# Kernel tuning notes

Measured on AMD Instinct MI355X. Metric: run time of the kernel, lower is better.

## Reference

```python
import jax, jax.numpy as jnp
import numpy as np

EPS = 1e-5


def _lstm(x, W_ih, W_hh, b_ih, b_hh):
    # x: [B, T, in]; torch LSTM gate order i, f, g, o. Returns (last h, last c).
    def step(carry, xt):
        h, c = carry
        z = xt @ W_ih.T + h @ W_hh.T + (b_ih + b_hh)  # [B, 4H]
        i, f, g, o = jnp.split(z, 4, axis=-1)
        c = jax.nn.sigmoid(f) * c + jax.nn.sigmoid(i) * jnp.tanh(g)
        h = jax.nn.sigmoid(o) * jnp.tanh(c)
        return (h, c), None
    h0 = jnp.zeros((x.shape[0], W_hh.shape[1]), x.dtype)
    (h, c), _ = jax.lax.scan(step, (h0, h0), jnp.swapaxes(x, 0, 1))
    return h, c


def _bn_train(x, g, b):
    # BatchNorm1d in training mode: batch stats, biased variance.
    m = x.mean(axis=0)
    v = x.var(axis=0)
    return g * (x - m) * jax.lax.rsqrt(v + EPS) + b


def _forward(agent_traj, neighbours, aW_ih, aW_hh, ab_ih, ab_hh,
             nW_ih, nW_hh, nb_ih, nb_hh, dW_ih, dW_hh, db_ih, db_hh,
             pW, pb, rW, rb, m1W, m1b, g1, be1, m2W, m2b, g2, be2,
             i1W, i1b, ig1, ib1, i2W, i2b, ig2, ib2, segment_ids):
    B = agent_traj.shape[0]
    # relative distance: neighbour last position - owning agent's last position
    rel = neighbours[:, -1, :] - agent_traj[segment_ids, -1, :]          # [N, 2]
    agent_h, agent_c = _lstm(agent_traj, aW_ih, aW_hh, ab_ih, ab_hh)     # [B, 64]
    neigh_h, _ = _lstm(neighbours, nW_ih, nW_hh, nb_ih, nb_hh)           # [N, 64]
    rel_emb = rel @ rW.T + rb                                            # [N, 64]
    x = jnp.concatenate([neigh_h, rel_emb], axis=1)                      # [N, 128]
    x = _bn_train(jax.nn.relu(x @ m1W.T + m1b), g1, be1)                 # [N, 512]
    x = _bn_train(jax.nn.relu(x @ m2W.T + m2b), g2, be2)                 # [N, 1024]
    # per-sample max pooling over each sample's neighbours (zeros if none)
    pooled = jax.ops.segment_max(x, segment_ids, num_segments=B)         # [B, 1024]
    counts = jax.ops.segment_sum(jnp.ones((x.shape[0],), x.dtype), segment_ids, num_segments=B)
    pooled = jnp.where(counts[:, None] > 0, pooled, jnp.zeros((), x.dtype))
    d = jnp.concatenate([pooled, agent_h], axis=1)                       # [B, 1088]
    d = _bn_train(jax.nn.relu(d @ i1W.T + i1b), ig1, ib1)                # [B, 1024]
    d = _bn_train(jax.nn.relu(d @ i2W.T + i2b), ig2, ib2)                # [B, 64]

    def dec_step(carry, _):
        h, c = carry
        z = h @ dW_ih.T + h @ dW_hh.T + (db_ih + db_hh)
        i, f, g, o = jnp.split(z, 4, axis=-1)
        c = jax.nn.sigmoid(f) * c + jax.nn.sigmoid(i) * jnp.tanh(g)
        h = jax.nn.sigmoid(o) * jnp.tanh(c)
        return (h, c), h
    _, hs = jax.lax.scan(dec_step, (d, agent_c), None, length=30)        # [30, B, 64]
    pred = jnp.einsum('tbh,oh->bto', hs, pW) + pb                        # [B, 30, 2]
    return pred


def setup_inputs() -> dict:
    B, T, N, Tn, H = 2048, 20, 32768, 20, 64
    key = jax.random.key(0)
    ki = iter(jax.random.split(key, 40))
    def rn(shape, s=0.1):
        return jax.random.normal(next(ki), shape, dtype=jnp.float32) * s
    inp = dict(
        agent_traj=rn((B, T, 2), 1.0),
        neighbours=rn((N, Tn, 2), 1.0),
        aW_ih=rn((4 * H, 2)), aW_hh=rn((4 * H, H)), ab_ih=rn((4 * H,)), ab_hh=rn((4 * H,)),
        nW_ih=rn((4 * H, 2)), nW_hh=rn((4 * H, H)), nb_ih=rn((4 * H,)), nb_hh=rn((4 * H,)),
        dW_ih=rn((4 * H, H)), dW_hh=rn((4 * H, H)), db_ih=rn((4 * H,)), db_hh=rn((4 * H,)),
        pW=rn((2, H)), pb=rn((2,)),
        rW=rn((H, 2)), rb=rn((H,)),
        m1W=rn((512, 128)), m1b=rn((512,)),
        g1=jnp.ones((512,), jnp.float32), be1=jnp.zeros((512,), jnp.float32),
        m2W=rn((1024, 512)), m2b=rn((1024,)),
        g2=jnp.ones((1024,), jnp.float32), be2=jnp.zeros((1024,), jnp.float32),
        i1W=rn((1024, 1088)), i1b=rn((1024,)),
        ig1=jnp.ones((1024,), jnp.float32), ib1=jnp.zeros((1024,), jnp.float32),
        i2W=rn((H, 1024)), i2b=rn((H,)),
        ig2=jnp.ones((H,), jnp.float32), ib2=jnp.zeros((H,), jnp.float32),
        segment_ids=jnp.sort(jax.random.randint(next(ki), (N,), 0, B)).astype(jnp.int32),
    )
    return inp


def reference(agent_traj, neighbours, aW_ih, aW_hh, ab_ih, ab_hh,
              nW_ih, nW_hh, nb_ih, nb_hh, dW_ih, dW_hh, db_ih, db_hh,
              pW, pb, rW, rb, m1W, m1b, g1, be1, m2W, m2b, g2, be2,
              i1W, i1b, ig1, ib1, i2W, i2b, ig2, ib2, segment_ids):
    return _forward(agent_traj, neighbours, aW_ih, aW_hh, ab_ih, ab_hh,
                    nW_ih, nW_hh, nb_ih, nb_hh, dW_ih, dW_hh, db_ih, db_hh,
                    pW, pb, rW, rb, m1W, m1b, g1, be1, m2W, m2b, g2, be2,
                    i1W, i1b, ig1, ib1, i2W, i2b, ig2, ib2, segment_ids)
```

## Files before the change

### kernel.cpp

```cpp
#include <hip/hip_runtime.h>

#define EPS_BN 1e-5f

typedef __attribute__((ext_vector_type(8))) short short8;
typedef __attribute__((ext_vector_type(4))) float f32x4;

__device__ __forceinline__ float fast_rcp(float x) { return __builtin_amdgcn_rcpf(x); }
__device__ __forceinline__ float sigmoid_f(float x) { return fast_rcp(1.0f + __expf(-x)); }
__device__ __forceinline__ float tanh_f(float x) { return 1.0f - 2.0f * fast_rcp(__expf(2.0f * x) + 1.0f); }

__device__ __forceinline__ unsigned short f2bf(float f) {
    unsigned u = __float_as_uint(f);
    u += 0x7FFFu + ((u >> 16) & 1u);
    return (unsigned short)(u >> 16);
}
__device__ __forceinline__ unsigned pk_bf(float a, float b) {
    return (unsigned)f2bf(a) | ((unsigned)f2bf(b) << 16);
}
__device__ __forceinline__ float bf_hi(float f) {
    return __uint_as_float((unsigned)f2bf(f) << 16);
}
__device__ __forceinline__ float bf2f(unsigned short u) {
    return __uint_as_float((unsigned)u << 16);
}

union AFrag { short e[8]; short8 v; };
union BFrag { uint4 u; short8 v; };

__global__ __launch_bounds__(256, 2) void lstm_mfma(
    const float* __restrict__ x,
    const float* __restrict__ W_ih,
    const float* __restrict__ W_hh,
    const float* __restrict__ b_ih,
    const float* __restrict__ b_hh,
    float* __restrict__ h_out,
    float* __restrict__ c_out,
    int T)
{
    __shared__ unsigned h_ex[2][2][16 * 52];

    const int tid  = threadIdx.x;
    const int w    = tid >> 6;
    const int lane = tid & 63;
    const int s    = lane & 15;
    const int q    = lane >> 4;

    short8 ahi[4][3], alo[4][3];
#pragma unroll
    for (int gt = 0; gt < 4; ++gt) {
        const int n = gt * 64 + w * 16 + s;
#pragma unroll
        for (int kc = 0; kc < 2; ++kc) {
            const float* src = &W_hh[n * 64 + kc * 32 + q * 8];
            float4 v0 = *(const float4*)src;
            float4 v1 = *(const float4*)(src + 4);
            float v[8] = {v0.x, v0.y, v0.z, v0.w, v1.x, v1.y, v1.z, v1.w};
            AFrag a, b;
#pragma unroll
            for (int j = 0; j < 8; ++j) {
                a.e[j] = (short)f2bf(v[j]);
                b.e[j] = (short)f2bf(v[j] - bf_hi(v[j]));
            }
            ahi[gt][kc] = a.v;
            alo[gt][kc] = b.v;
        }
        AFrag a2, b2;
#pragma unroll
        for (int j = 0; j < 8; ++j) { a2.e[j] = 0; b2.e[j] = 0; }
        if (q == 0) {
            const float wi0 = W_ih[n * 2 + 0];
            const float wi1 = W_ih[n * 2 + 1];
            const float bs  = b_ih[n] + b_hh[n];
            a2.e[0] = (short)f2bf(wi0); b2.e[0] = (short)f2bf(wi0 - bf_hi(wi0));
            a2.e[1] = (short)f2bf(wi1); b2.e[1] = (short)f2bf(wi1 - bf_hi(wi1));
            a2.e[2] = (short)f2bf(bs);  b2.e[2] = (short)f2bf(bs  - bf_hi(bs));
        }
        ahi[gt][2] = a2.v;
        alo[gt][2] = b2.v;
    }

    for (int i = tid; i < 2 * 2 * 16 * 52; i += 256) (&h_ex[0][0][0])[i] = 0u;
    __syncthreads();
    if (tid < 16) {
        h_ex[0][0][tid * 52 + 33] = pk_bf(1.0f, 0.0f);
        h_ex[1][0][tid * 52 + 33] = pk_bf(1.0f, 0.0f);
        float2 xv = *(const float2*)&x[((long)blockIdx.x * 16 + tid) * (long)(T * 2)];
        h_ex[0][0][tid * 52 + 32] = pk_bf(xv.x, xv.y);
        h_ex[0][1][tid * 52 + 32] = pk_bf(xv.x - bf_hi(xv.x), xv.y - bf_hi(xv.y));
    }
    __syncthreads();

    float creg[4] = {0.f, 0.f, 0.f, 0.f};

    for (int t = 0; t < T; ++t) {
        const int rb = t & 1, wb = rb ^ 1;
        BFrag bhi[3], blo[3];
#pragma unroll
        for (int kc = 0; kc < 3; ++kc) {
            const int off = s * 52 + kc * 16 + (q >> 1) * 8 + (q & 1) * 4;
            bhi[kc].u = *(const uint4*)&h_ex[rb][0][off];
            blo[kc].u = *(const uint4*)&h_ex[rb][1][off];
        }

        f32x4 acc[4];
#pragma unroll
        for (int gt = 0; gt < 4; ++gt) acc[gt] = (f32x4)0.f;

#pragma unroll
        for (int kc = 0; kc < 3; ++kc) {
            const short8 bh = bhi[kc].v;
            const short8 bl = blo[kc].v;
#pragma unroll
            for (int gt = 0; gt < 4; ++gt) {
                f32x4 a = acc[gt];
                a = __builtin_amdgcn_mfma_f32_16x16x32_bf16(ahi[gt][kc], bh, a, 0, 0, 0);
                a = __builtin_amdgcn_mfma_f32_16x16x32_bf16(ahi[gt][kc], bl, a, 0, 0, 0);
                a = __builtin_amdgcn_mfma_f32_16x16x32_bf16(alo[gt][kc], bh, a, 0, 0, 0);
                acc[gt] = a;
            }
        }

        float hval[4];
#pragma unroll
        for (int r = 0; r < 4; ++r) {
            const float c = fmaf(sigmoid_f(acc[1][r]), creg[r],
                                 sigmoid_f(acc[0][r]) * tanh_f(acc[2][r]));
            creg[r] = c;
            hval[r] = sigmoid_f(acc[3][r]) * tanh_f(c);
        }
        {
            const int w0 = s * 52 + w * 8 + q * 2;
            h_ex[wb][0][w0]     = pk_bf(hval[0], hval[1]);
            h_ex[wb][0][w0 + 1] = pk_bf(hval[2], hval[3]);
            h_ex[wb][1][w0]     = pk_bf(hval[0] - bf_hi(hval[0]), hval[1] - bf_hi(hval[1]));
            h_ex[wb][1][w0 + 1] = pk_bf(hval[2] - bf_hi(hval[2]), hval[3] - bf_hi(hval[3]));
        }
        if (tid < 16 && t + 1 < T) {
            float2 xv = *(const float2*)&x[((long)blockIdx.x * 16 + tid) * (long)(T * 2) + (t + 1) * 2];
            h_ex[wb][0][tid * 52 + 32] = pk_bf(xv.x, xv.y);
            h_ex[wb][1][tid * 52 + 32] = pk_bf(xv.x - bf_hi(xv.x), xv.y - bf_hi(xv.y));
        }
        if (t == T - 1) {
            const long seq = (long)blockIdx.x * 16 + s;
            const int j0 = w * 16 + q * 4;
            *(float4*)&h_out[seq * 64 + j0] = make_float4(hval[0], hval[1], hval[2], hval[3]);
            if (c_out)
                *(float4*)&c_out[seq * 64 + j0] = make_float4(creg[0], creg[1], creg[2], creg[3]);
        }
        __syncthreads();
    }
}

__global__ __launch_bounds__(256) void build_x0(
    const float* __restrict__ neigh_h, const float* __restrict__ neighbours,
    const float* __restrict__ agent_traj, const int* __restrict__ seg,
    const float* __restrict__ rW, const float* __restrict__ rb,
    unsigned short* __restrict__ x0hi, unsigned short* __restrict__ x0lo, int T)
{
    const long n = (long)blockIdx.x * 2 + (threadIdx.x >> 7);
    const int j = threadIdx.x & 127;
    float v;
    if (j < 64) {
        v = neigh_h[n*64 + j];
    } else {
        const int o = j - 64;
        const int sid = seg[n];
        const float ra = neighbours[n*(long)(T*2) + (T-1)*2 + 0] - agent_traj[(long)sid*(T*2) + (T-1)*2 + 0];
        const float rbv= neighbours[n*(long)(T*2) + (T-1)*2 + 1] - agent_traj[(long)sid*(T*2) + (T-1)*2 + 1];
        v = fmaf(rW[o*2+0], ra, fmaf(rW[o*2+1], rbv, rb[o]));
    }
    x0hi[n*128 + j] = f2bf(v);
    x0lo[n*128 + j] = f2bf(v - bf_hi(v));
}

__global__ __launch_bounds__(64) void prep_wfrag(
    const float* __restrict__ W, const float* __restrict__ sc, int K,
    unsigned short* __restrict__ Whi, unsigned short* __restrict__ Wlo)
{
    const int nKc = K >> 5;
    const int blk = blockIdx.x;
    const int ti = blk / nKc, kc = blk - ti * nKc;
    const int l = threadIdx.x;
    const int n = ti * 16 + (l & 15);
    const int k0 = kc * 32 + (l >> 4) * 8;
    const long ob = ((long)blk * 64 + l) * 8;
#pragma unroll
    for (int j = 0; j < 8; ++j) {
        float v = W[(long)n * K + k0 + j];
        if (sc) v *= sc[k0 + j];
        Whi[ob + j] = f2bf(v);
        Wlo[ob + j] = f2bf(v - bf_hi(v));
    }
}

__global__ __launch_bounds__(64) void prep_bias(
    const float* __restrict__ W, const float* __restrict__ sh,
    const float* __restrict__ b, int K, float* __restrict__ bout)
{
    const int n = blockIdx.x;
    const int l = threadIdx.x;
    float s = 0.f;
    if (sh)
        for (int k = l; k < K; k += 64) s += sh[k] * W[(long)n * K + k];
#pragma unroll
    for (int m = 32; m >= 1; m >>= 1) s += __shfl_xor(s, m, 64);
    if (l == 0) bout[n] = b[n] + s;
}

__global__ __launch_bounds__(256, 2) void gemm_split(
    const unsigned short* __restrict__ Ahi,
    const unsigned short* __restrict__ Alo,
    const unsigned short* __restrict__ Whi,
    const unsigned short* __restrict__ Wlo,
    const float* __restrict__ bias,
    float* __restrict__ Yf,
    unsigned short* __restrict__ Yhi,
    unsigned short* __restrict__ Ylo,
    float* __restrict__ accum,
    const int* __restrict__ segp,
    float* __restrict__ poolmax,
    int M, int K, int O)
{
    __shared__ unsigned short As[2][2][128 * 56];
    __shared__ int segl[128];
    const int t = threadIdx.x;
    const int lane = t & 63;
    const int w = t >> 6;
    const int wm = w & 1, wn = w >> 1;

    const int nx = gridDim.x;
    const int flat = blockIdx.y * nx + blockIdx.x;
    const int grp = flat / (8 * nx);
    const int loc = flat - grp * (8 * nx);
    const int m0 = (grp * 8 + (loc & 7)) * 128;
    const int n0 = (loc >> 3) * 128;
    const int nKc = K >> 5;

    f32x4 acc[4][4];
#pragma unroll
    for (int mt = 0; mt < 4; ++mt)
#pragma unroll
    for (int nt = 0; nt < 4; ++nt) acc[mt][nt] = (f32x4)0.f;

    const long aoff = (long)(m0 + (t >> 1)) * K + (t & 1) * 16;
    const unsigned short* aph = Ahi + aoff;
    const unsigned short* apl = Alo + aoff;
    const int so = (t >> 1) * 56 + (t & 1) * 16;
    const int arow = wm * 64 + (lane & 15);
    const int acol = (lane >> 4) * 8;
    const long bt0 = (long)((n0 >> 4) + wn * 4);

    uint4 rah0, rah1, ral0, ral1;
    auto loadAreg = [&](int kc) {
        rah0 = *(const uint4*)(aph + kc * 32);
        rah1 = *(const uint4*)(aph + kc * 32 + 8);
        ral0 = *(const uint4*)(apl + kc * 32);
        ral1 = *(const uint4*)(apl + kc * 32 + 8);
    };
    auto storeAs = [&](int buf) {
        *(uint4*)&As[buf][0][so] = rah0; *(uint4*)&As[buf][0][so + 8] = rah1;
        *(uint4*)&As[buf][1][so] = ral0; *(uint4*)&As[buf][1][so + 8] = ral1;
    };
    auto loadB = [&](BFrag* bh, BFrag* bl, int kc) {
#pragma unroll
        for (int nt = 0; nt < 4; ++nt) {
            const long fb = ((bt0 + nt) * nKc + kc) * 512 + lane * 8;
            bh[nt].u = *(const uint4*)(Whi + fb);
            bl[nt].u = *(const uint4*)(Wlo + fb);
        }
    };
    auto compute = [&](int buf, BFrag* bh, BFrag* bl) {
        BFrag afh[4], afl[4];
#pragma unroll
        for (int mt = 0; mt < 4; ++mt) {
            afh[mt].u = *(const uint4*)&As[buf][0][(arow + mt * 16) * 56 + acol];
            afl[mt].u = *(const uint4*)&As[buf][1][(arow + mt * 16) * 56 + acol];
        }
#pragma unroll
        for (int nt = 0; nt < 4; ++nt)
#pragma unroll
        for (int mt = 0; mt < 4; ++mt) {
            f32x4 a = acc[mt][nt];
            a = __builtin_amdgcn_mfma_f32_16x16x32_bf16(afh[mt].v, bh[nt].v, a, 0, 0, 0);
            a = __builtin_amdgcn_mfma_f32_16x16x32_bf16(afh[mt].v, bl[nt].v, a, 0, 0, 0);
            a = __builtin_amdgcn_mfma_f32_16x16x32_bf16(afl[mt].v, bh[nt].v, a, 0, 0, 0);
            acc[mt][nt] = a;
        }
    };

    BFrag bh0[4], bl0[4], bh1[4], bl1[4];
    loadAreg(0);
    loadB(bh0, bl0, 0);
    storeAs(0);
    __syncthreads();
    for (int kc = 0; kc < nKc; kc += 2) {
        loadAreg(kc + 1);
        loadB(bh1, bl1, kc + 1);
        compute(0, bh0, bl0);
        storeAs(1);
        __syncthreads();
        if (kc + 2 < nKc) {
            loadAreg(kc + 2);
            loadB(bh0, bl0, kc + 2);
        }
        compute(1, bh1, bl1);
        if (kc + 2 < nKc) {
            storeAs(0);
            __syncthreads();
        }
    }

    if (segp) {
        __syncthreads();
        if (t < 128) segl[t] = segp[m0 + t];
        __syncthreads();
    }

    const int cn = lane & 15, cq = lane >> 4;
#pragma unroll
    for (int nt = 0; nt < 4; ++nt) {
        const int n = n0 + wn * 64 + nt * 16 + cn;
        const float bs = bias[n];
        float s = 0.f, ssq = 0.f;
#pragma unroll
        for (int mt = 0; mt < 4; ++mt) {
            const int mb = wm * 64 + mt * 16 + cq * 4;
            float vmax = 0.f; int sid = -1;
#pragma unroll
            for (int r = 0; r < 4; ++r) {
                const float v = fmaxf(acc[mt][nt][r] + bs, 0.f);
                s += v; ssq += v * v;
                if (segp) {
                    const int sr = segl[mb + r];
                    if (r == 0) { vmax = v; sid = sr; }
                    else if (sr == sid) { vmax = fmaxf(vmax, v); }
                    else {
                        if (vmax > 0.f)
                            atomicMax((int*)&poolmax[(long)sid * O + n], __float_as_int(vmax));
                        sid = sr; vmax = v;
                    }
                } else if (Yf) {
                    Yf[(long)(m0 + mb + r) * O + n] = v;
                } else {
                    const long idx = (long)(m0 + mb + r) * O + n;
                    Yhi[idx] = f2bf(v);
                    Ylo[idx] = f2bf(v - bf_hi(v));
                }
            }
            if (segp && vmax > 0.f)
                atomicMax((int*)&poolmax[(long)sid * O + n], __float_as_int(vmax));
        }
        if (accum) {
            s   += __shfl_xor(s, 16, 64);   ssq += __shfl_xor(ssq, 16, 64);
            s   += __shfl_xor(s, 32, 64);   ssq += __shfl_xor(ssq, 32, 64);
            if (cq == 0) {
                atomicAdd(&accum[n], s);
                atomicAdd(&accum[O + n], ssq);
            }
        }
    }
}

__global__ __launch_bounds__(256) void colstats(
    const float* __restrict__ Y, int M, int O, int chunkRows,
    float* __restrict__ accum)
{
    const int c = blockIdx.x * 64 + (threadIdx.x & 63);
    const int rgrp = threadIdx.x >> 6;
    const int r0 = blockIdx.y * chunkRows;
    int rend = r0 + chunkRows; if (rend > M) rend = M;
    float s = 0.f, ss = 0.f;
    for (int r = r0 + rgrp; r < rend; r += 4) {
        const float v = Y[(long)r*O + c];
        s += v; ss += v*v;
    }
    __shared__ float l1[256], l2[256];
    l1[threadIdx.x] = s; l2[threadIdx.x] = ss;
    __syncthreads();
    if (threadIdx.x < 64) {
        const int c2 = blockIdx.x * 64 + threadIdx.x;
        s  = l1[threadIdx.x] + l1[threadIdx.x+64] + l1[threadIdx.x+128] + l1[threadIdx.x+192];
        ss = l2[threadIdx.x] + l2[threadIdx.x+64] + l2[threadIdx.x+128] + l2[threadIdx.x+192];
        atomicAdd(&accum[c2], s);
        atomicAdd(&accum[O + c2], ss);
    }
}

__global__ __launch_bounds__(256) void bn_finalize(
    const float* __restrict__ accum, const float* __restrict__ g,
    const float* __restrict__ be, int O, float invM,
    float* __restrict__ scale, float* __restrict__ shift)
{
    const int o = blockIdx.x * 256 + threadIdx.x;
    if (o < O) {
        const float mean = accum[o] * invM;
        const float var  = accum[O + o] * invM - mean * mean;
        const float sc   = g[o] * rsqrtf(var + EPS_BN);
        scale[o] = sc;
        shift[o] = be[o] - mean * sc;
    }
}

__global__ __launch_bounds__(256) void build_d0(
    const float* __restrict__ poolraw, const float* __restrict__ agent_h,
    const int* __restrict__ seg, int N,
    const float* __restrict__ sc2, const float* __restrict__ sh2,
    unsigned short* __restrict__ d0hi, unsigned short* __restrict__ d0lo)
{
    const int b = blockIdx.x;
    int l = 0, h = N;
    while (l < h) { const int mid = (l + h) >> 1; if (seg[mid] < b) l = mid + 1; else h = mid; }
    const bool nonempty = (l < N) && (seg[l] == b);
    for (int c = threadIdx.x; c < 1088; c += 256) {
        float v;
        if (c < 1024) {
            v = nonempty ? fmaf(sc2[c], poolraw[(long)b*1024 + c], sh2[c]) : 0.f;
        } else {
            v = agent_h[(long)b*64 + (c - 1024)];
        }
        d0hi[(long)b*1088 + c] = f2bf(v);
        d0lo[(long)b*1088 + c] = f2bf(v - bf_hi(v));
    }
}

__global__ __launch_bounds__(256) void gemm_i2_part(
    const float* __restrict__ A,
    const float* __restrict__ W,
    const float* __restrict__ ascale, const float* __restrict__ ashift,
    float* __restrict__ part, int M, int K, int kchunk)
{
    __shared__ float As[16][132];
    __shared__ float Bs[16][68];
    const int t = threadIdx.x;
    const int m0 = blockIdx.x * 128;
    const int ks = blockIdx.y;
    const int kbeg = ks * kchunk;
    const int kend = kbeg + kchunk;
    const int tm = (t & 15) * 8;
    const int tn = (t >> 4) * 4;
    const int ar = t >> 1;
    const int ac = (t & 1) * 8;
    const int br = t >> 2;
    const int bc = (t & 3) * 4;

    float acc[8][4];
#pragma unroll
    for (int i = 0; i < 8; ++i)
#pragma unroll
    for (int j = 0; j < 4; ++j) acc[i][j] = 0.f;

    for (int k0 = kbeg; k0 < kend; k0 += 16) {
        float4 a0 = *(const float4*)&A[(long)(m0+ar)*K + k0 + ac];
        float4 a1 = *(const float4*)&A[(long)(m0+ar)*K + k0 + ac + 4];
        float4 s0 = *(const float4*)&ascale[k0 + ac];
        float4 s1 = *(const float4*)&ascale[k0 + ac + 4];
        float4 h0 = *(const float4*)&ashift[k0 + ac];
        float4 h1 = *(const float4*)&ashift[k0 + ac + 4];
        a0.x = fmaf(a0.x, s0.x, h0.x); a0.y = fmaf(a0.y, s0.y, h0.y);
        a0.z = fmaf(a0.z, s0.z, h0.z); a0.w = fmaf(a0.w, s0.w, h0.w);
        a1.x = fmaf(a1.x, s1.x, h1.x); a1.y = fmaf(a1.y, s1.y, h1.y);
        a1.z = fmaf(a1.z, s1.z, h1.z); a1.w = fmaf(a1.w, s1.w, h1.w);
        float4 b0 = *(const float4*)&W[(long)br*K + k0 + bc];
        __syncthreads();
        As[ac+0][ar] = a0.x; As[ac+1][ar] = a0.y; As[ac+2][ar] = a0.z; As[ac+3][ar] = a0.w;
        As[ac+4][ar] = a1.x; As[ac+5][ar] = a1.y; As[ac+6][ar] = a1.z; As[ac+7][ar] = a1.w;
        Bs[bc+0][br] = b0.x; Bs[bc+1][br] = b0.y; Bs[bc+2][br] = b0.z; Bs[bc+3][br] = b0.w;
        __syncthreads();
#pragma unroll
        for (int kk = 0; kk < 16; ++kk) {
            float av[8], bv[4];
            *(float4*)&av[0] = *(const float4*)&As[kk][tm];
            *(float4*)&av[4] = *(const float4*)&As[kk][tm + 4];
            *(float4*)&bv[0] = *(const float4*)&Bs[kk][tn];
#pragma unroll
            for (int i = 0; i < 8; ++i)
#pragma unroll
            for (int j = 0; j < 4; ++j)
                acc[i][j] = fmaf(av[i], bv[j], acc[i][j]);
        }
    }

    float* po = part + (long)ks * M * 64;
#pragma unroll
    for (int i = 0; i < 8; ++i)
        *(float4*)&po[(long)(m0 + tm + i) * 64 + tn] = *(float4*)&acc[i][0];
}

__global__ __launch_bounds__(256) void i2_finish(
    const float* __restrict__ part, const float* __restrict__ bias,
    int M, int KS, float* __restrict__ t2)
{
    const long idx = (long)blockIdx.x * 256 + threadIdx.x;
    if (idx < (long)M * 64) {
        float s = 0.f;
        for (int ks = 0; ks < KS; ++ks) s += part[(long)ks * M * 64 + idx];
        t2[idx] = fmaxf(s + bias[idx & 63], 0.f);
    }
}

__global__ __launch_bounds__(256) void prep_dec(
    const float* __restrict__ dW_ih, const float* __restrict__ dW_hh,
    const float* __restrict__ db_ih, const float* __restrict__ db_hh,
    float* __restrict__ Wc, float* __restrict__ bc)
{
    const int idx = blockIdx.x * 256 + threadIdx.x;
    if (idx < 256*64) Wc[idx] = dW_ih[idx] + dW_hh[idx];
    else if (idx < 256*64 + 256) bc[idx - 256*64] = db_ih[idx - 256*64] + db_hh[idx - 256*64];
}

__global__ __launch_bounds__(256) void decoder_kernel(
    const float* __restrict__ t2, const float* __restrict__ sc4,
    const float* __restrict__ sh4, const float* __restrict__ agent_c,
    const float* __restrict__ Wc, const float* __restrict__ bc,
    const float* __restrict__ pW, const float* __restrict__ pb,
    float* __restrict__ pred )
{
    __shared__ float h_lds[2][64];
    __shared__ float zg_lds[2][64];
    __shared__ float zo_lds[2][64];
    const int t = threadIdx.x;
    const int lane = t & 63;
    const int wave = t >> 6;
    const int s = wave >> 1;
    const int role = wave & 1;
    const long seq = (long)blockIdx.x * 2 + s;

    const int r0 = role * 128 + lane;
    const int r1 = r0 + 64;
    float w0[64], w1[64];
#pragma unroll
    for (int k = 0; k < 64; k += 4) {
        float4 va = *(const float4*)&Wc[r0 * 64 + k];
        w0[k] = va.x; w0[k+1] = va.y; w0[k+2] = va.z; w0[k+3] = va.w;
        float4 vb = *(const float4*)&Wc[r1 * 64 + k];
        w1[k] = vb.x; w1[k+1] = vb.y; w1[k+2] = vb.z; w1[k+3] = vb.w;
    }
    const float bias0 = bc[r0];
    const float bias1 = bc[r1];
    const float pw0 = pW[lane], pw1 = pW[64 + lane];
    const float pb0 = pb[0], pb1 = pb[1];

    float c = agent_c[seq*64 + lane];
    if (role == 0)
        h_lds[s][lane] = fmaf(sc4[lane], t2[seq*64 + lane], sh4[lane]);
    __syncthreads();
    float hv = h_lds[s][lane];

    for (int step = 0; step < 30; ++step) {
        float z0 = bias0, z1 = bias1;
#pragma unroll
        for (int k = 0; k < 64; ++k) {
            float hk = __int_as_float(__builtin_amdgcn_readlane(__float_as_int(hv), k));
            z0 = fmaf(hk, w0[k], z0);
            z1 = fmaf(hk, w1[k], z1);
        }
        if (role == 1) { zg_lds[s][lane] = z0; zo_lds[s][lane] = z1; }
        __syncthreads();
        if (role == 0) {
            const float ig = sigmoid_f(z0);
            const float fg = sigmoid_f(z1);
            const float gg = tanh_f(zg_lds[s][lane]);
            const float og = sigmoid_f(zo_lds[s][lane]);
            c = fmaf(fg, c, ig * gg);
            h_lds[s][lane] = og * tanh_f(c);
        }
        __syncthreads();
        hv = h_lds[s][lane];
        if (role == 0) {
            float p0 = hv * pw0;
            float p1 = hv * pw1;
#pragma unroll
            for (int m = 32; m >= 1; m >>= 1) {
                p0 += __shfl_xor(p0, m, 64);
                p1 += __shfl_xor(p1, m, 64);
            }
            if (lane == 0) {
                pred[seq*60 + step*2 + 0] = p0 + pb0;
                pred[seq*60 + step*2 + 1] = p1 + pb1;
            }
        }
    }
}

extern "C" void kernel_launch(void* const* d_in, const int* in_sizes, int n_in,
                              void* d_out, int out_size, void* d_ws, size_t ws_size,
                              hipStream_t stream)
{
    const float* agent_traj = (const float*)d_in[0];
    const float* neighbours = (const float*)d_in[1];
    const float* aW_ih = (const float*)d_in[2];
    const float* aW_hh = (const float*)d_in[3];
    const float* ab_ih = (const float*)d_in[4];
    const float* ab_hh = (const float*)d_in[5];
    const float* nW_ih = (const float*)d_in[6];
    const float* nW_hh = (const float*)d_in[7];
    const float* nb_ih = (const float*)d_in[8];
    const float* nb_hh = (const float*)d_in[9];
    const float* dW_ih = (const float*)d_in[10];
    const float* dW_hh = (const float*)d_in[11];
    const float* db_ih = (const float*)d_in[12];
    const float* db_hh = (const float*)d_in[13];
    const float* pW = (const float*)d_in[14];
    const float* pb = (const float*)d_in[15];
    const float* rW = (const float*)d_in[16];
    const float* rb = (const float*)d_in[17];
    const float* m1W = (const float*)d_in[18];
    const float* m1b = (const float*)d_in[19];
    const float* g1  = (const float*)d_in[20];
    const float* be1 = (const float*)d_in[21];
    const float* m2W = (const float*)d_in[22];
    const float* m2b = (const float*)d_in[23];
    const float* g2  = (const float*)d_in[24];
    const float* be2 = (const float*)d_in[25];
    const float* i1W = (const float*)d_in[26];
    const float* i1b = (const float*)d_in[27];
    const float* ig1 = (const float*)d_in[28];
    const float* ib1 = (const float*)d_in[29];
    const float* i2W = (const float*)d_in[30];
    const float* i2b = (const float*)d_in[31];
    const float* ig2 = (const float*)d_in[32];
    const float* ib2 = (const float*)d_in[33];
    const int*   seg = (const int*)d_in[34];
    float* pred = (float*)d_out;

    const int B = 2048, T = 20, N = 32768;

    char* p = (char*)d_ws;
    auto alloc = [&](size_t bytes) -> char* {
        char* r = p; p += (bytes + 255) & ~(size_t)255; return r;
    };
    float* agent_h = (float*)alloc((size_t)B*64*4);
    float* agent_c = (float*)alloc((size_t)B*64*4);
    char* neigh_region = alloc((size_t)N*64*4);
    unsigned short* x0hi = (unsigned short*)alloc((size_t)N*128*2);
    unsigned short* x0lo = (unsigned short*)alloc((size_t)N*128*2);
    char* y1hi_region  = alloc((size_t)N*512*2);
    unsigned short* y1lo = (unsigned short*)alloc((size_t)N*512*2);
    float* poolraw = (float*)alloc((size_t)B*1024*4);
    float* accAll = (float*)alloc((size_t)(1024+2048+2048+128)*4);
    float* acc1 = accAll;
    float* acc2 = accAll + 1024;
    float* acc3 = accAll + 3072;
    float* acc4 = accAll + 5120;
    float* sc1 = (float*)alloc(512*4);  float* sh1 = (float*)alloc(512*4);
    float* sc2 = (float*)alloc(1024*4); float* sh2 = (float*)alloc(1024*4);
    float* sc3 = (float*)alloc(1024*4); float* sh3 = (float*)alloc(1024*4);
    float* sc4 = (float*)alloc(64*4);   float* sh4 = (float*)alloc(64*4);
    float* Wc = (float*)alloc(256*64*4);
    float* bc = (float*)alloc(256*4);
    unsigned short* W1hi = (unsigned short*)alloc((size_t)512*128*2);
    unsigned short* W1lo = (unsigned short*)alloc((size_t)512*128*2);
    unsigned short* W2hi = (unsigned short*)alloc((size_t)1024*512*2);
    unsigned short* W2lo = (unsigned short*)alloc((size_t)1024*512*2);
    unsigned short* Wi1hi = (unsigned short*)alloc((size_t)1024*1088*2);
    unsigned short* Wi1lo = (unsigned short*)alloc((size_t)1024*1088*2);
    float* b1f = (float*)alloc(512*4);
    float* b2f = (float*)alloc(1024*4);
    float* bi1f = (float*)alloc(1024*4);
    float* i2part = (float*)alloc((size_t)8*B*64*4);

    float* neigh_h = (float*)neigh_region;
    float* t1      = (float*)neigh_region;
    unsigned short* y1hi = (unsigned short*)y1hi_region;
    unsigned short* d0hi = (unsigned short*)y1hi_region;
    unsigned short* d0lo = d0hi + (size_t)B*1088;
    float* t2 = (float*)(y1hi_region + (size_t)2*B*1088*2);

    hipMemsetAsync(accAll, 0, (1024+2048+2048+128)*sizeof(float), stream);
    hipMemsetAsync(poolraw, 0, (size_t)B*1024*4, stream);

    prep_wfrag<<<(512/16)*(128/32), 64, 0, stream>>>(m1W, nullptr, 128, W1hi, W1lo);
    prep_bias<<<512, 64, 0, stream>>>(m1W, nullptr, m1b, 128, b1f);
    prep_wfrag<<<(1024/16)*(1088/32), 64, 0, stream>>>(i1W, nullptr, 1088, Wi1hi, Wi1lo);
    prep_bias<<<1024, 64, 0, stream>>>(i1W, nullptr, i1b, 1088, bi1f);
    prep_dec<<<65, 256, 0, stream>>>(dW_ih, dW_hh, db_ih, db_hh, Wc, bc);

    lstm_mfma<<<B/16, 256, 0, stream>>>(agent_traj, aW_ih, aW_hh, ab_ih, ab_hh,
                                        agent_h, agent_c, T);
    lstm_mfma<<<N/16, 256, 0, stream>>>(neighbours, nW_ih, nW_hh, nb_ih, nb_hh,
                                        neigh_h, nullptr, T);
    build_x0<<<N/2, 256, 0, stream>>>(neigh_h, neighbours, agent_traj, seg, rW, rb,
                                      x0hi, x0lo, T);

    gemm_split<<<dim3(512/128, N/128), 256, 0, stream>>>(
        x0hi, x0lo, W1hi, W1lo, b1f, nullptr, y1hi, y1lo, acc1,
        nullptr, nullptr, N, 128, 512);
    bn_finalize<<<2, 256, 0, stream>>>(acc1, g1, be1, 512, 1.0f/N, sc1, sh1);

    prep_wfrag<<<(1024/16)*(512/32), 64, 0, stream>>>(m2W, sc1, 512, W2hi, W2lo);
    prep_bias<<<1024, 64, 0, stream>>>(m2W, sh1, m2b, 512, b2f);

    gemm_split<<<dim3(1024/128, N/128), 256, 0, stream>>>(
        y1hi, y1lo, W2hi, W2lo, b2f, nullptr, nullptr, nullptr, acc2,
        seg, poolraw, N, 512, 1024);
    bn_finalize<<<4, 256, 0, stream>>>(acc2, g2, be2, 1024, 1.0f/N, sc2, sh2);

    build_d0<<<B, 256, 0, stream>>>(poolraw, agent_h, seg, N, sc2, sh2, d0hi, d0lo);

    gemm_split<<<dim3(1024/128, B/128), 256, 0, stream>>>(
        d0hi, d0lo, Wi1hi, Wi1lo, bi1f, t1, nullptr, nullptr, acc3,
        nullptr, nullptr, B, 1088, 1024);
    bn_finalize<<<4, 256, 0, stream>>>(acc3, ig1, ib1, 1024, 1.0f/B, sc3, sh3);

    gemm_i2_part<<<dim3(B/128, 8), 256, 0, stream>>>(t1, i2W, sc3, sh3, i2part,
                                                     B, 1024, 128);
    i2_finish<<<(B*64)/256, 256, 0, stream>>>(i2part, i2b, B, 8, t2);
    colstats<<<dim3(1, 8), 256, 0, stream>>>(t2, B, 64, 256, acc4);
    bn_finalize<<<1, 256, 0, stream>>>(acc4, ig2, ib2, 64, 1.0f/B, sc4, sh4);

    decoder_kernel<<<B/2, 256, 0, stream>>>(t2, sc4, sh4, agent_c, Wc, bc, pW, pb, pred);
}
```

Before: 641.4 us.

## Load A fragments directly from global memory, dropping LDS double buffering in split GEMM

The split-bf16 GEMM kernel no longer stages A tiles through double-buffered shared memory with barriers. Each wave now reads its A fragments straight from global memory inside a simple k-loop, alongside the B fragments. This removes LDS traffic and block-wide __syncthreads, but it also drops the software prefetch that overlapped the next k-chunk's loads with the current MFMAs. A rows are now read redundantly by the two wn waves, and the column-strided reads may coalesce poorly.

After: 756.2 us. +17.9%, slower.

```diff
diff --git a/kernel.cpp b/kernel.cpp
--- a/kernel.cpp
+++ b/kernel.cpp
@@ -221,7 +221,6 @@
     float* __restrict__ poolmax,
     int M, int K, int O)
 {
-    __shared__ unsigned short As[2][2][128 * 56];
     __shared__ int segl[128];
     const int t = threadIdx.x;
     const int lane = t & 63;
@@ -242,39 +241,24 @@
 #pragma unroll
     for (int nt = 0; nt < 4; ++nt) acc[mt][nt] = (f32x4)0.f;
 
-    const long aoff = (long)(m0 + (t >> 1)) * K + (t & 1) * 16;
-    const unsigned short* aph = Ahi + aoff;
-    const unsigned short* apl = Alo + aoff;
-    const int so = (t >> 1) * 56 + (t & 1) * 16;
-    const int arow = wm * 64 + (lane & 15);
+    const int arow = m0 + wm * 64 + (lane & 15);
     const int acol = (lane >> 4) * 8;
     const long bt0 = (long)((n0 >> 4) + wn * 4);
 
-    uint4 rah0, rah1, ral0, ral1;
-    auto loadAreg = [&](int kc) {
-        rah0 = *(const uint4*)(aph + kc * 32);
-        rah1 = *(const uint4*)(aph + kc * 32 + 8);
-        ral0 = *(const uint4*)(apl + kc * 32);
-        ral1 = *(const uint4*)(apl + kc * 32 + 8);
-    };
-    auto storeAs = [&](int buf) {
-        *(uint4*)&As[buf][0][so] = rah0; *(uint4*)&As[buf][0][so + 8] = rah1;
-        *(uint4*)&As[buf][1][so] = ral0; *(uint4*)&As[buf][1][so + 8] = ral1;
-    };
-    auto loadB = [&](BFrag* bh, BFrag* bl, int kc) {
+    for (int kc = 0; kc < nKc; ++kc) {
+        BFrag afh[4], afl[4], bh[4], bl[4];
+        const long kb = (long)kc * 32 + acol;
+#pragma unroll
+        for (int mt = 0; mt < 4; ++mt) {
+            const long ao = (long)(arow + mt * 16) * K + kb;
+            afh[mt].u = *(const uint4*)(Ahi + ao);
+            afl[mt].u = *(const uint4*)(Alo + ao);
+        }
 #pragma unroll
         for (int nt = 0; nt < 4; ++nt) {
             const long fb = ((bt0 + nt) * nKc + kc) * 512 + lane * 8;
             bh[nt].u = *(const uint4*)(Whi + fb);
             bl[nt].u = *(const uint4*)(Wlo + fb);
-        }
-    };
-    auto compute = [&](int buf, BFrag* bh, BFrag* bl) {
-        BFrag afh[4], afl[4];
-#pragma unroll
-        for (int mt = 0; mt < 4; ++mt) {
-            afh[mt].u = *(const uint4*)&As[buf][0][(arow + mt * 16) * 56 + acol];
-            afl[mt].u = *(const uint4*)&As[buf][1][(arow + mt * 16) * 56 + acol];
         }
 #pragma unroll
         for (int nt = 0; nt < 4; ++nt)
@@ -286,32 +270,9 @@
             a = __builtin_amdgcn_mfma_f32_16x16x32_bf16(afl[mt].v, bh[nt].v, a, 0, 0, 0);
             acc[mt][nt] = a;
         }
-    };
-
-    BFrag bh0[4], bl0[4], bh1[4], bl1[4];
-    loadAreg(0);
-    loadB(bh0, bl0, 0);
-    storeAs(0);
-    __syncthreads();
-    for (int kc = 0; kc < nKc; kc += 2) {
-        loadAreg(kc + 1);
-        loadB(bh1, bl1, kc + 1);
-        compute(0, bh0, bl0);
-        storeAs(1);
-        __syncthreads();
-        if (kc + 2 < nKc) {
-            loadAreg(kc + 2);
-            loadB(bh0, bl0, kc + 2);
-        }
-        compute(1, bh1, bl1);
-        if (kc + 2 < nKc) {
-            storeAs(0);
-            __syncthreads();
-        }
     }
 
     if (segp) {
-        __syncthreads();
         if (t < 128) segl[t] = segp[m0 + t];
         __syncthreads();
     }
```
